# Kernel tuning notes

Hardware: AMD Instinct MI355X
Metric: run time of the kernel (lower is better)

Reference implementation:

```python
import jax, jax.numpy as jnp
import numpy as np

NUM_CLASSES = 80
ALPHA = 1.0
BETA = 6.0
EPS = 1e-9      # assigner eps
IOU_EPS = 1e-7  # bbox_iou eps


def _iou_xyxy(b1, b2):
    # b1: (B, A, 1, 4), b2: (B, 1, M, 4) -> IoU (B, A, M); matches bbox_iou(xywh=False)
    b1x1, b1y1, b1x2, b1y2 = (b1[..., 0], b1[..., 1], b1[..., 2], b1[..., 3])
    b2x1, b2y1, b2x2, b2y2 = (b2[..., 0], b2[..., 1], b2[..., 2], b2[..., 3])
    w1, h1 = b1x2 - b1x1, b1y2 - b1y1 + IOU_EPS
    w2, h2 = b2x2 - b2x1, b2y2 - b2y1 + IOU_EPS
    iw = jnp.clip(jnp.minimum(b1x2, b2x2) - jnp.maximum(b1x1, b2x1), 0)
    ih = jnp.clip(jnp.minimum(b1y2, b2y2) - jnp.maximum(b1y1, b2y1), 0)
    inter = iw * ih
    union = w1 * h1 + w2 * h2 - inter + IOU_EPS
    return inter / union


def _select_highest_overlaps(mask_pos, overlaps, M):
    # Always apply the dedup branch; it is a no-op when no anchor has >1 gt.
    fg = mask_pos.sum(-1)                                   # (B, A)
    multi = fg > 1
    is_max = jax.nn.one_hot(overlaps.argmax(-1), M, dtype=mask_pos.dtype)  # (B, A, M)
    mask_pos = jnp.where(multi[..., None], is_max, mask_pos)
    fg = mask_pos.sum(-1)
    tgt = mask_pos.argmax(-1).astype(jnp.int32)             # (B, A)
    return tgt, fg, mask_pos


def _forward(pd_scores, pd_bboxes, anc_points, gt_labels, gt_bboxes, mask_gt):
    B, A, C = pd_scores.shape
    M = gt_bboxes.shape[1]
    f = pd_scores.dtype
    mgt_b = mask_gt.astype(bool)                            # (B, M)
    mgt_f = mask_gt.astype(f)

    # --- box metrics ---
    overlaps = jnp.clip(_iou_xyxy(pd_bboxes[:, :, None, :], gt_bboxes[:, None, :, :]), 0)  # (B,A,M)
    idx = jnp.broadcast_to(gt_labels[:, None, :].astype(jnp.int32), (B, A, M))
    cls_scores = jnp.take_along_axis(pd_scores, idx, axis=-1)                              # (B,A,M)
    align_metric = cls_scores ** ALPHA * overlaps ** BETA

    # --- anchors inside gt boxes ---
    lt = anc_points[None, :, None, :] - gt_bboxes[:, None, :, :2]   # (B,A,M,2)
    rb = gt_bboxes[:, None, :, 2:] - anc_points[None, :, None, :]
    mask_in_gts = jnp.concatenate([lt, rb], -1).min(-1) > EPS       # (B,A,M) bool
    mask_pos = mask_in_gts.astype(f) * mgt_f[:, None, :]

    # --- fix 1 (vectorized: each (b,gt) iteration only touches its own column) ---
    need1 = mgt_b & (mask_pos.sum(1) == 0)                          # (B,M)
    has_in = mask_in_gts.any(1)                                     # (B,M)
    best1 = jnp.where(has_in, (overlaps * mask_in_gts).argmax(1), overlaps.argmax(1))  # (B,M)
    oh1 = jax.nn.one_hot(best1, A, dtype=f).transpose(0, 2, 1)      # (B,A,M)
    mask_pos = jnp.maximum(mask_pos, oh1 * need1[:, None, :].astype(f))

    tgt, fg, mask_pos = _select_highest_overlaps(mask_pos, overlaps, M)

    # --- fix 2: sequential per-gt reassignment (order-dependent -> lax.scan) ---
    anchor_ids = jnp.arange(A)
    gt_ids = jnp.arange(M)

    def step(carry, g):
        mp, tgi, fgm = carry
        assigned = jnp.any((fgm > 0) & (tgi == g), axis=1)          # (B,)
        need = jnp.take(mgt_b, g, axis=1) & (~assigned)             # (B,)
        best = jnp.take(overlaps, g, axis=2).argmax(1)              # (B,)
        oh_b = anchor_ids[None, :] == best[:, None]                 # (B,A) bool
        upd = need[:, None] & oh_b                                  # (B,A)
        col = (gt_ids == g)[None, None, :]
        mp = jnp.where(upd[:, :, None] & col, jnp.asarray(1, mp.dtype), mp)
        tgi = jnp.where(upd, g, tgi)
        fgm = jnp.where(upd, jnp.asarray(1, fgm.dtype), fgm)
        return (mp, tgi, fgm), None

    (mask_pos, tgt, fg), _ = jax.lax.scan(step, (mask_pos, tgt, fg), jnp.arange(M, dtype=jnp.int32))
    tgt, fg, mask_pos = _select_highest_overlaps(mask_pos, overlaps, M)

    # --- targets ---
    tl = jnp.take_along_axis(gt_labels.astype(jnp.int32), tgt, axis=1)   # (B,A)
    tl = jnp.clip(tl, 0, NUM_CLASSES)
    tb = jnp.take_along_axis(gt_bboxes, tgt[..., None], axis=1)          # (B,A,4)
    ts = jax.nn.one_hot(tl, C, dtype=f)                                  # (B,A,C)
    ts = jnp.where(fg[..., None] > 0, ts, jnp.asarray(0, f))

    # --- normalize scores by task-aligned metric ---
    am = align_metric * mask_pos
    pam = am.max(-1, keepdims=True)                                      # (B,A,1)
    pov = (overlaps * mask_pos).max(-1, keepdims=True)
    norm = (am * pov / (pam + EPS)).max(-1, keepdims=True)               # (B,A,1)
    ts = ts * norm
    return tl, tb, ts, fg > 0, tgt


def setup_inputs() -> dict:
    key = jax.random.key(0)
    B, C, M, IMG = 32, NUM_CLASSES, 32, 640
    ks = jax.random.split(key, 8)
    # YOLO-style anchor grid: strides 8/16/32 -> 80^2 + 40^2 + 20^2 = 8400 points
    pts = []
    for s in (8, 16, 32):
        n = IMG // s
        xs = (np.arange(n, dtype=np.float32) + 0.5) * s
        gy, gx = np.meshgrid(xs, xs, indexing="ij")
        pts.append(np.stack([gx.ravel(), gy.ravel()], -1))
    anc_points = jnp.asarray(np.concatenate(pts, 0))                     # (8400, 2)
    A = anc_points.shape[0]
    pd_scores = jax.random.uniform(ks[0], (B, A, C), dtype=jnp.float32)  # sigmoid-like scores
    wh_p = jax.random.uniform(ks[1], (B, A, 2), minval=16.0, maxval=256.0)
    ctr_p = anc_points[None] + jax.random.normal(ks[2], (B, A, 2)) * 8.0
    pd_bboxes = jnp.concatenate([ctr_p - wh_p / 2, ctr_p + wh_p / 2], -1)
    ctr_g = jax.random.uniform(ks[3], (B, M, 2), minval=60.0, maxval=580.0)
    wh_g = jax.random.uniform(ks[4], (B, M, 2), minval=24.0, maxval=240.0)
    gt_bboxes = jnp.concatenate([ctr_g - wh_g / 2, ctr_g + wh_g / 2], -1)
    gt_labels = jax.random.randint(ks[5], (B, M), 0, C, dtype=jnp.int32)
    n_gt = jax.random.randint(ks[6], (B, 1), 1, M + 1)
    mask_gt = jnp.arange(M)[None, :] < n_gt                              # (B, M) bool
    return dict(pd_scores=pd_scores, pd_bboxes=pd_bboxes, anc_points=anc_points,
                gt_labels=gt_labels, gt_bboxes=gt_bboxes, mask_gt=mask_gt)


def reference(pd_scores, pd_bboxes, anc_points, gt_labels, gt_bboxes, mask_gt):
    return _forward(pd_scores, pd_bboxes, anc_points, gt_labels, gt_bboxes, mask_gt)
```

## Files before the change

kernel.cpp:

```cpp
#include <hip/hip_runtime.h>


#define EPS_IN   1e-9f
#define IOU_EPS  1e-7f

__device__ __forceinline__ float iou_pair(const float4 p, const float4 g) {
#pragma clang fp contract(off)
    float w1 = p.z - p.x;
    float h1 = (p.w - p.y) + IOU_EPS;
    float w2 = g.z - g.x;
    float h2 = (g.w - g.y) + IOU_EPS;
    float iw = fminf(p.z, g.z) - fmaxf(p.x, g.x);
    iw = fmaxf(iw, 0.0f);
    float ih = fminf(p.w, g.w) - fmaxf(p.y, g.y);
    ih = fmaxf(ih, 0.0f);
    float inter = iw * ih;
    float uni = w1 * h1 + w2 * h2 - inter + IOU_EPS;
    float r = inter / uni;
    return fmaxf(r, 0.0f);
}

__device__ __forceinline__ int detect_mode(const void* mg, int nw) {
    const unsigned* w = (const unsigned*)mg;
    int lane = threadIdx.x & 63;
    int badI = 0, badF = 0;
    for (int i = lane; i < nw; i += 64) {
        unsigned v = w[i];
        badI |= (v > 1u);
        badF |= (v != 0u && v != 0x3F800000u);
    }
    unsigned long long bI = __ballot(badI != 0);
    unsigned long long bF = __ballot(badF != 0);
    return bI ? (bF ? 2 : 1) : 0;
}

__device__ __forceinline__ bool mask_at(const void* mg, int mode, int idx) {
    if (mode == 0) return ((const int*)mg)[idx] != 0;
    if (mode == 1) return ((const float*)mg)[idx] != 0.0f;
    return ((const unsigned char*)mg)[idx] != 0;
}

__global__ void k_phase1(const float4* __restrict__ pdb, const float2* __restrict__ anc,
                         const float4* __restrict__ gtb, const void* mg, int nw,
                         unsigned long long* __restrict__ colKey,
                         unsigned char* __restrict__ needByte,
                         unsigned* __restrict__ rowbits0, short* __restrict__ tgt0,
                         int* __restrict__ cntChunk,
                         int A, int M, int nCh) {
    int b = blockIdx.y, tid = threadIdx.x;
    int mode = detect_mode(mg, nw);
    size_t bA = (size_t)b * A;

    if ((int)blockIdx.x < M) {
        int m = blockIdx.x;
        if (!mask_at(mg, mode, b * M + m)) return;
        float4 g = gtb[b * M + m];
        unsigned long long key = 0ull;
        int hasin = 0;
        for (int a = tid; a < A; a += 256) {
            float v = iou_pair(pdb[bA + a], g);
            unsigned long long k =
                ((unsigned long long)__float_as_uint(v) << 32) | (0xFFFFFFFFu - (unsigned)a);
            if (k > key) key = k;
            float2 an = anc[a];
            float mn = fminf(fminf(an.x - g.x, an.y - g.y), fminf(g.z - an.x, g.w - an.y));
            hasin |= (mn > EPS_IN);
        }
        __shared__ unsigned long long skey[4];
        __shared__ int sin_[4];
        int lane = tid & 63, wid = tid >> 6;
        for (int off = 32; off; off >>= 1) {
            unsigned long long o = __shfl_down(key, off);
            if (o > key) key = o;
            hasin |= __shfl_down(hasin, off);
        }
        if (lane == 0) { skey[wid] = key; sin_[wid] = hasin; }
        __syncthreads();
        if (tid == 0) {
            for (int i = 1; i < 4; i++) { if (skey[i] > key) key = skey[i]; hasin |= sin_[i]; }
            colKey[b * M + m] = key;
            needByte[b * M + m] = hasin ? 0 : 1;
        }
    } else {
        int ch = blockIdx.x - M;
        int a = ch * 256 + tid;
        __shared__ float4 sg[32];
        __shared__ unsigned char smg[32];
        __shared__ int shist[32];
        if (tid < M) {
            sg[tid]  = gtb[b * M + tid];
            smg[tid] = mask_at(mg, mode, b * M + tid) ? 1 : 0;
        }
        if (tid < 32) shist[tid] = 0;
        __syncthreads();
        if (a < A) {
            float2 an = anc[a];
            unsigned bits = 0u;
            for (int m = 0; m < M; m++) {
                float4 g = sg[m];
                float mn = fminf(fminf(an.x - g.x, an.y - g.y), fminf(g.z - an.x, g.w - an.y));
                if (mn > EPS_IN && smg[m]) bits |= (1u << m);
            }
            rowbits0[bA + a] = bits;
            int pc = __popc(bits);
            int t;
            if (pc > 1) {
                float4 p = pdb[bA + a];
                float bv = -1.0f; int bm = 0;
                for (int m = 0; m < M; m++) {
                    float v = iou_pair(p, sg[m]);
                    if (v > bv) { bv = v; bm = m; }
                }
                t = bm;
            } else if (pc == 1) t = __ffs(bits) - 1;
            else t = -1;
            tgt0[bA + a] = (short)t;
            if (t >= 0) atomicAdd(&shist[t], 1);
        }
        __syncthreads();
        if (tid < 32) cntChunk[((size_t)b * nCh + ch) * 32 + tid] = shist[tid];
    }
}

__global__ void k_final(const float* __restrict__ pds, const float4* __restrict__ pdb,
                        const float4* __restrict__ gtb, const int* __restrict__ gtl,
                        const void* mg, int nw,
                        const unsigned long long* __restrict__ colKey,
                        const unsigned char* __restrict__ needByte,
                        const unsigned* __restrict__ rowbits0,
                        const short* __restrict__ tgt0,
                        const int* __restrict__ cntChunk,
                        float* __restrict__ out,
                        int A, int M, int C, int B, int nCh) {
    int b = blockIdx.y;
    int base = blockIdx.x * 256;
    int tid = threadIdx.x;
    int mode = detect_mode(mg, nw);
    size_t bA = (size_t)b * A;
    __shared__ float4 sg[32];
    __shared__ int slab[32];
    __shared__ int ovrA[64];
    __shared__ unsigned ovrBits[64];
    __shared__ int sNov;
    __shared__ float snorm[256];
    __shared__ int stl[256];
    if (tid < M) { sg[tid] = gtb[b * M + tid]; slab[tid] = gtl[b * M + tid]; }
    __syncthreads();

    if (tid < 64) {
        bool mv = false, needv = false;
        int best = -1, c0 = 0;
        if (tid < M) mv = mask_at(mg, mode, b * M + tid);
        if (mv) {
            unsigned long long key = colKey[b * M + tid];
            best = (int)(0xFFFFFFFFu - (unsigned)(key & 0xFFFFFFFFull));
            needv = (needByte[b * M + tid] != 0);
        }
        if (tid < 32) {
            for (int ch = 0; ch < nCh; ch++)
                c0 += cntChunk[((size_t)b * nCh + ch) * 32 + tid];
        }
        int myPre = (mv && best >= 0) ? (int)tgt0[bA + best] : -1;
        unsigned maskbits = (unsigned)__ballot(mv);
        unsigned needBits = (unsigned)__ballot(needv);
        unsigned myEq = 0u;
        for (int g2 = 0; g2 < 32; g2++) {
            int bb = __shfl(best, g2);
            if (bb == best) myEq |= (1u << g2);
        }
        int nov = 0;
        unsigned rem = needBits;
        while (rem) {
            int gl = __ffs(rem) - 1;
            unsigned em = __shfl(myEq, gl) & needBits;
            rem &= ~em;
            int aF = __shfl(best, gl);
            unsigned addb = em;
            unsigned bits0 = rowbits0[bA + aF];
            unsigned bits1 = bits0 | addb;
            int t1;
            if (__popc(bits1) > 1) {
                float4 p = pdb[bA + aF];
                unsigned long long kk = 0ull;
                if (tid < M) {
                    float v = iou_pair(p, sg[tid]);
                    kk = ((unsigned long long)__float_as_uint(v) << 32) |
                         (0xFFFFFFFFu - (unsigned)tid);
                }
                for (int off = 32; off; off >>= 1) {
                    unsigned long long o = __shfl_down(kk, off);
                    if (o > kk) kk = o;
                }
                kk = __shfl(kk, 0);
                t1 = (int)(0xFFFFFFFFu - (unsigned)(kk & 0xFFFFFFFFull));
            } else {
                t1 = __ffs(bits1) - 1;
            }
            int t0a = __shfl(myPre, gl);
            if (tid == t0a && t0a >= 0) c0--;
            if (tid == t1) c0++;
            if (best == aF) myPre = t1;
            if (tid == 0) { ovrA[nov] = aF; ovrBits[nov] = addb; }
            nov++;
        }
        unsigned applied = 0u;
        for (int g = 0; g < M; g++) {
            int cg = __shfl(c0, g);
            if (((maskbits >> g) & 1u) && cg == 0) {
                int aa      = __shfl(best, g);
                unsigned em = __shfl(myEq, g);
                unsigned x  = applied & em;
                int old;
                if (x) old = 31 - __clz(x);
                else   old = __shfl(myPre, g);
                if (tid == old) c0--;
                if (tid == g)   c0++;
                applied |= (1u << g);
                if (tid == 0) { ovrA[nov] = aa; ovrBits[nov] = 1u << g; }
                nov++;
            }
        }
        if (tid == 0) sNov = nov;
    }
    __syncthreads();

    int a = base + tid;
    size_t BA = (size_t)B * A;
    int nov = sNov;
    if (a < A) {
        size_t idx = bA + a;
        unsigned bits = rowbits0[idx];
        for (int j = 0; j < nov; j++)
            if (ovrA[j] == a) bits |= ovrBits[j];
        int pc = __popc(bits);
        int tgt, fg; float ov = 0.0f;
        float4 p = pdb[idx];
        if (pc > 1) {
            float bv = -1.0f; int bm = 0;
            for (int m = 0; m < M; m++) {
                float v = iou_pair(p, sg[m]);
                if (v > bv) { bv = v; bm = m; }
            }
            tgt = bm; fg = 1; ov = bv;
        } else if (pc == 1) {
            tgt = __ffs(bits) - 1; fg = 1;
            ov = iou_pair(p, sg[tgt]);
        } else { tgt = 0; fg = 0; }
        int lab = slab[tgt];
        int tl = min(max(lab, 0), C);
        float norm = 0.0f;
        if (fg) {
            int li = (lab >= 0 && lab < C) ? lab : 0;
            float cls = pds[idx * (size_t)C + li];
            float ov6 = powf(ov, 6.0f);
            float v = cls * ov6;
            norm = v * ov / (v + 1e-9f);
        }
        out[idx] = (float)tl;
        ((float4*)(out + BA))[idx] = sg[tgt];
        out[BA * (size_t)(5 + C) + idx] = fg ? 1.0f : 0.0f;
        out[BA * (size_t)(6 + C) + idx] = (float)tgt;
        snorm[tid] = norm;
        stl[tid] = tl;
    }
    __syncthreads();
    int cntA = min(256, A - base);
    int rowf4 = C >> 2;
    int nf4 = cntA * rowf4;
    float4* tsb = (float4*)(out + BA * 5 + (bA + base) * C);
    int q = 256 / rowf4, r = 256 - q * rowf4;
    int row = tid / rowf4;
    int c4  = tid - row * rowf4;
    for (int i = tid; i < nf4; i += 256) {
        float nv = snorm[row];
        int tl   = stl[row];
        int cb = c4 * 4;
        float4 v;
        v.x = (tl == cb + 0) ? nv : 0.0f;
        v.y = (tl == cb + 1) ? nv : 0.0f;
        v.z = (tl == cb + 2) ? nv : 0.0f;
        v.w = (tl == cb + 3) ? nv : 0.0f;
        tsb[i] = v;
        row += q; c4 += r;
        if (c4 >= rowf4) { c4 -= rowf4; row++; }
    }
}

extern "C" void kernel_launch(void* const* d_in, const int* in_sizes, int n_in,
                              void* d_out, int out_size, void* d_ws, size_t ws_size,
                              hipStream_t stream) {
    const float*  pd_scores = (const float*)d_in[0];
    const float4* pd_bboxes = (const float4*)d_in[1];
    const float2* anc       = (const float2*)d_in[2];
    const int*    gt_labels = (const int*)d_in[3];
    const float4* gt_bboxes = (const float4*)d_in[4];
    const void*   mask_gt   = d_in[5];

    int A = in_sizes[2] / 2;
    int B = in_sizes[1] / (A * 4);
    int M = in_sizes[3] / B;
    int C = (int)((long long)in_sizes[0] / ((long long)B * A));
    int nCh = (A + 255) / 256;
    int nw = (B * M) / 4; if (nw > 256) nw = 256;

    char* wp = (char*)d_ws;
    auto carve = [&](size_t bytes) -> char* {
        char* r = wp; wp += (bytes + 255) & ~(size_t)255; return r;
    };
    unsigned* rowbits0         = (unsigned*)carve((size_t)B * A * 4);
    short* tgt0                = (short*)carve((size_t)B * A * 2);
    unsigned long long* colKey = (unsigned long long*)carve((size_t)B * M * 8);
    unsigned char* needByte    = (unsigned char*)carve((size_t)B * M);
    int* cntChunk              = (int*)carve((size_t)B * nCh * 32 * 4);

    float* out = (float*)d_out;

    k_phase1<<<dim3(M + nCh, B), 256, 0, stream>>>(pd_bboxes, anc, gt_bboxes, mask_gt, nw,
                                                   colKey, needByte, rowbits0, tgt0,
                                                   cntChunk, A, M, nCh);
    k_final<<<dim3(nCh, B), 256, 0, stream>>>(pd_scores, pd_bboxes, gt_bboxes, gt_labels,
                                              mask_gt, nw, colKey, needByte, rowbits0,
                                              tgt0, cntChunk, out, A, M, C, B, nCh);
}
```

Measured before the change: 53.33 us.

## Fuse per-gt column argmax into anchor-chunk blocks and reuse target in final

Removes the separate per-gt blocks that each scanned all anchors. Every anchor-chunk block now computes all 32 IoUs once, keeps them in registers, and emits per-chunk column max keys and in-box bitmasks, which the final kernel reduces across chunks. The final kernel also reuses the stored tgt0 plus a small precomputed override table instead of recomputing the in-box bits and argmax per anchor. The cost is more wavefront reductions per chunk (32 shuffle-reduce loops), higher register pressure, and an extra serial reduction over chunks in the final kernel.

```diff
diff --git a/kernel.cpp b/kernel.cpp
--- a/kernel.cpp
+++ b/kernel.cpp
@@ -42,91 +42,95 @@
 
 __global__ void k_phase1(const float4* __restrict__ pdb, const float2* __restrict__ anc,
                          const float4* __restrict__ gtb, const void* mg, int nw,
-                         unsigned long long* __restrict__ colKey,
-                         unsigned char* __restrict__ needByte,
+                         unsigned long long* __restrict__ colChunk,
+                         unsigned* __restrict__ hasinChunk,
                          unsigned* __restrict__ rowbits0, short* __restrict__ tgt0,
                          int* __restrict__ cntChunk,
                          int A, int M, int nCh) {
-    int b = blockIdx.y, tid = threadIdx.x;
+    int b = blockIdx.y, ch = blockIdx.x, tid = threadIdx.x;
+    int lane = tid & 63, wid = tid >> 6;
     int mode = detect_mode(mg, nw);
+    __shared__ float4 sg[32];
+    __shared__ unsigned sMask;
+    __shared__ float swv[4][32];
+    __shared__ int   swa[4][32];
+    __shared__ unsigned swh[4];
+    __shared__ int shist[32];
+    if (tid < 32) {
+        sg[tid] = (tid < M) ? gtb[b * M + tid] : make_float4(0.f, 0.f, 0.f, 0.f);
+        shist[tid] = 0;
+    }
+    if (tid < 64) {
+        bool mv = (tid < M) && mask_at(mg, mode, b * M + tid);
+        unsigned mb = (unsigned)__ballot(mv);
+        if (tid == 0) sMask = mb;
+    }
+    __syncthreads();
+    unsigned maskb = sMask;
     size_t bA = (size_t)b * A;
-
-    if ((int)blockIdx.x < M) {
-        int m = blockIdx.x;
-        if (!mask_at(mg, mode, b * M + m)) return;
-        float4 g = gtb[b * M + m];
-        unsigned long long key = 0ull;
-        int hasin = 0;
-        for (int a = tid; a < A; a += 256) {
-            float v = iou_pair(pdb[bA + a], g);
-            unsigned long long k =
-                ((unsigned long long)__float_as_uint(v) << 32) | (0xFFFFFFFFu - (unsigned)a);
-            if (k > key) key = k;
-            float2 an = anc[a];
-            float mn = fminf(fminf(an.x - g.x, an.y - g.y), fminf(g.z - an.x, g.w - an.y));
-            hasin |= (mn > EPS_IN);
-        }
-        __shared__ unsigned long long skey[4];
-        __shared__ int sin_[4];
-        int lane = tid & 63, wid = tid >> 6;
-        for (int off = 32; off; off >>= 1) {
-            unsigned long long o = __shfl_down(key, off);
-            if (o > key) key = o;
-            hasin |= __shfl_down(hasin, off);
-        }
-        if (lane == 0) { skey[wid] = key; sin_[wid] = hasin; }
-        __syncthreads();
-        if (tid == 0) {
-            for (int i = 1; i < 4; i++) { if (skey[i] > key) key = skey[i]; hasin |= sin_[i]; }
-            colKey[b * M + m] = key;
-            needByte[b * M + m] = hasin ? 0 : 1;
-        }
-    } else {
-        int ch = blockIdx.x - M;
-        int a = ch * 256 + tid;
-        __shared__ float4 sg[32];
-        __shared__ unsigned char smg[32];
-        __shared__ int shist[32];
-        if (tid < M) {
-            sg[tid]  = gtb[b * M + tid];
-            smg[tid] = mask_at(mg, mode, b * M + tid) ? 1 : 0;
-        }
-        if (tid < 32) shist[tid] = 0;
-        __syncthreads();
-        if (a < A) {
-            float2 an = anc[a];
-            unsigned bits = 0u;
-            for (int m = 0; m < M; m++) {
-                float4 g = sg[m];
-                float mn = fminf(fminf(an.x - g.x, an.y - g.y), fminf(g.z - an.x, g.w - an.y));
-                if (mn > EPS_IN && smg[m]) bits |= (1u << m);
-            }
-            rowbits0[bA + a] = bits;
-            int pc = __popc(bits);
-            int t;
-            if (pc > 1) {
-                float4 p = pdb[bA + a];
-                float bv = -1.0f; int bm = 0;
-                for (int m = 0; m < M; m++) {
-                    float v = iou_pair(p, sg[m]);
-                    if (v > bv) { bv = v; bm = m; }
-                }
-                t = bm;
-            } else if (pc == 1) t = __ffs(bits) - 1;
-            else t = -1;
-            tgt0[bA + a] = (short)t;
-            if (t >= 0) atomicAdd(&shist[t], 1);
-        }
-        __syncthreads();
-        if (tid < 32) cntChunk[((size_t)b * nCh + ch) * 32 + tid] = shist[tid];
+    int a = ch * 256 + tid;
+    bool valid = a < A;
+    float4 p = make_float4(0.f, 0.f, 0.f, 0.f);
+    float2 an = make_float2(0.f, 0.f);
+    if (valid) { p = pdb[bA + a]; an = anc[a]; }
+    float v[32];
+    unsigned inbox = 0u;
+#pragma unroll
+    for (int m = 0; m < 32; m++) {
+        float4 g = sg[m];
+        bool ok = valid && (m < M);
+        v[m] = ok ? iou_pair(p, g) : -1.0f;
+        float mn = fminf(fminf(an.x - g.x, an.y - g.y), fminf(g.z - an.x, g.w - an.y));
+        if (ok && mn > EPS_IN) inbox |= (1u << m);
+    }
+    if (valid) {
+        unsigned bits = inbox & maskb;
+        int pc = __popc(bits);
+        int t = -1;
+        if (pc > 1) {
+            float bv = -0.5f; int bm = 0;
+#pragma unroll
+            for (int m = 0; m < 32; m++) { if (v[m] > bv) { bv = v[m]; bm = m; } }
+            t = bm;
+        } else if (pc == 1) t = __ffs(bits) - 1;
+        rowbits0[bA + a] = bits;
+        tgt0[bA + a] = (short)t;
+        if (t >= 0) atomicAdd(&shist[t], 1);
+    } else if (a < ((A + 255) & ~255)) {
+    }
+    unsigned hw = inbox;
+    for (int off = 32; off; off >>= 1) hw |= __shfl_xor(hw, off);
+    if (lane == 0) swh[wid] = hw;
+#pragma unroll
+    for (int m = 0; m < 32; m++) {
+        float vm = v[m];
+        for (int off = 32; off; off >>= 1) vm = fmaxf(vm, __shfl_xor(vm, off));
+        unsigned long long eq = __ballot(v[m] == vm);
+        if (lane == 0) {
+            swv[wid][m] = vm;
+            swa[wid][m] = ch * 256 + wid * 64 + (__ffsll((unsigned long long)eq) - 1);
+        }
+    }
+    __syncthreads();
+    if (tid < 32) {
+        float bv = swv[0][tid]; int ba = swa[0][tid];
+        for (int w = 1; w < 4; w++) {
+            float vv = swv[w][tid]; int aa = swa[w][tid];
+            if (vv > bv || (vv == bv && aa < ba)) { bv = vv; ba = aa; }
+        }
+        unsigned long long key = (bv < 0.0f) ? 0ull :
+            (((unsigned long long)__float_as_uint(bv) << 32) | (0xFFFFFFFFu - (unsigned)ba));
+        colChunk[((size_t)b * nCh + ch) * 32 + tid] = key;
+        cntChunk[((size_t)b * nCh + ch) * 32 + tid] = shist[tid];
+        if (tid == 0) hasinChunk[b * nCh + ch] = swh[0] | swh[1] | swh[2] | swh[3];
     }
 }
 
 __global__ void k_final(const float* __restrict__ pds, const float4* __restrict__ pdb,
                         const float4* __restrict__ gtb, const int* __restrict__ gtl,
                         const void* mg, int nw,
-                        const unsigned long long* __restrict__ colKey,
-                        const unsigned char* __restrict__ needByte,
+                        const unsigned long long* __restrict__ colChunk,
+                        const unsigned* __restrict__ hasinChunk,
                         const unsigned* __restrict__ rowbits0,
                         const short* __restrict__ tgt0,
                         const int* __restrict__ cntChunk,
@@ -140,27 +144,32 @@
     __shared__ float4 sg[32];
     __shared__ int slab[32];
     __shared__ int ovrA[64];
-    __shared__ unsigned ovrBits[64];
+    __shared__ unsigned ovrAdd[64];
+    __shared__ short ovrT[64];
     __shared__ int sNov;
     __shared__ float snorm[256];
     __shared__ int stl[256];
-    if (tid < M) { sg[tid] = gtb[b * M + tid]; slab[tid] = gtl[b * M + tid]; }
+    if (tid < 32) {
+        sg[tid]   = (tid < M) ? gtb[b * M + tid] : make_float4(0.f, 0.f, 0.f, 0.f);
+        slab[tid] = (tid < M) ? gtl[b * M + tid] : 0;
+    }
     __syncthreads();
 
     if (tid < 64) {
-        bool mv = false, needv = false;
-        int best = -1, c0 = 0;
-        if (tid < M) mv = mask_at(mg, mode, b * M + tid);
-        if (mv) {
-            unsigned long long key = colKey[b * M + tid];
-            best = (int)(0xFFFFFFFFu - (unsigned)(key & 0xFFFFFFFFull));
-            needv = (needByte[b * M + tid] != 0);
-        }
+        bool mv = (tid < M) && mask_at(mg, mode, b * M + tid);
+        unsigned long long key = 0ull;
+        int c0 = 0; unsigned horAll = 0u;
         if (tid < 32) {
-            for (int ch = 0; ch < nCh; ch++)
+            for (int ch = 0; ch < nCh; ch++) {
+                unsigned long long k2 = colChunk[((size_t)b * nCh + ch) * 32 + tid];
+                if (k2 > key) key = k2;
                 c0 += cntChunk[((size_t)b * nCh + ch) * 32 + tid];
-        }
-        int myPre = (mv && best >= 0) ? (int)tgt0[bA + best] : -1;
+                horAll |= hasinChunk[b * nCh + ch];
+            }
+        }
+        int best = mv ? (int)(0xFFFFFFFFu - (unsigned)(key & 0xFFFFFFFFull)) : -1;
+        bool needv = mv && !((horAll >> tid) & 1u);
+        int myPre = (best >= 0) ? (int)tgt0[bA + best] : -1;
         unsigned maskbits = (unsigned)__ballot(mv);
         unsigned needBits = (unsigned)__ballot(needv);
         unsigned myEq = 0u;
@@ -176,15 +185,14 @@
             rem &= ~em;
             int aF = __shfl(best, gl);
             unsigned addb = em;
-            unsigned bits0 = rowbits0[bA + aF];
-            unsigned bits1 = bits0 | addb;
+            unsigned bits1 = rowbits0[bA + aF] | addb;
             int t1;
             if (__popc(bits1) > 1) {
                 float4 p = pdb[bA + aF];
                 unsigned long long kk = 0ull;
                 if (tid < M) {
-                    float v = iou_pair(p, sg[tid]);
-                    kk = ((unsigned long long)__float_as_uint(v) << 32) |
+                    float vv = iou_pair(p, sg[tid]);
+                    kk = ((unsigned long long)__float_as_uint(vv) << 32) |
                          (0xFFFFFFFFu - (unsigned)tid);
                 }
                 for (int off = 32; off; off >>= 1) {
@@ -200,7 +208,7 @@
             if (tid == t0a && t0a >= 0) c0--;
             if (tid == t1) c0++;
             if (best == aF) myPre = t1;
-            if (tid == 0) { ovrA[nov] = aF; ovrBits[nov] = addb; }
+            if (tid == 0) { ovrA[nov] = aF; ovrAdd[nov] = addb; }
             nov++;
         }
         unsigned applied = 0u;
@@ -216,50 +224,68 @@
                 if (tid == old) c0--;
                 if (tid == g)   c0++;
                 applied |= (1u << g);
-                if (tid == 0) { ovrA[nov] = aa; ovrBits[nov] = 1u << g; }
+                if (tid == 0) { ovrA[nov] = aa; ovrAdd[nov] = 1u << g; }
                 nov++;
             }
         }
         if (tid == 0) sNov = nov;
     }
     __syncthreads();
+    if (tid < 64) {
+        int nov2 = sNov;
+        for (int j = 0; j < nov2; j++) {
+            int aj = ovrA[j];
+            unsigned addT = 0u;
+            for (int k = 0; k < nov2; k++) if (ovrA[k] == aj) addT |= ovrAdd[k];
+            unsigned bt = rowbits0[bA + aj] | addT;
+            int tf;
+            if (__popc(bt) > 1) {
+                float4 p = pdb[bA + aj];
+                unsigned long long kk = 0ull;
+                if (tid < M) {
+                    float vv = iou_pair(p, sg[tid]);
+                    kk = ((unsigned long long)__float_as_uint(vv) << 32) |
+                         (0xFFFFFFFFu - (unsigned)tid);
+                }
+                for (int off = 32; off; off >>= 1) {
+                    unsigned long long o = __shfl_down(kk, off);
+                    if (o > kk) kk = o;
+                }
+                kk = __shfl(kk, 0);
+                tf = (int)(0xFFFFFFFFu - (unsigned)(kk & 0xFFFFFFFFull));
+            } else {
+                tf = __ffs(bt) - 1;
+            }
+            if (tid == 0) ovrT[j] = (short)tf;
+        }
+    }
+    __syncthreads();
 
     int a = base + tid;
     size_t BA = (size_t)B * A;
-    int nov = sNov;
     if (a < A) {
         size_t idx = bA + a;
-        unsigned bits = rowbits0[idx];
-        for (int j = 0; j < nov; j++)
-            if (ovrA[j] == a) bits |= ovrBits[j];
-        int pc = __popc(bits);
-        int tgt, fg; float ov = 0.0f;
-        float4 p = pdb[idx];
-        if (pc > 1) {
-            float bv = -1.0f; int bm = 0;
-            for (int m = 0; m < M; m++) {
-                float v = iou_pair(p, sg[m]);
-                if (v > bv) { bv = v; bm = m; }
-            }
-            tgt = bm; fg = 1; ov = bv;
-        } else if (pc == 1) {
-            tgt = __ffs(bits) - 1; fg = 1;
-            ov = iou_pair(p, sg[tgt]);
-        } else { tgt = 0; fg = 0; }
-        int lab = slab[tgt];
+        int t = (int)tgt0[idx];
+        int nov2 = sNov;
+        for (int j = 0; j < nov2; j++)
+            if (ovrA[j] == a) t = (int)ovrT[j];
+        int fg = (t >= 0);
+        int tgtO = fg ? t : 0;
+        int lab = slab[tgtO];
         int tl = min(max(lab, 0), C);
         float norm = 0.0f;
         if (fg) {
+            float ov = iou_pair(pdb[idx], sg[t]);
             int li = (lab >= 0 && lab < C) ? lab : 0;
             float cls = pds[idx * (size_t)C + li];
             float ov6 = powf(ov, 6.0f);
-            float v = cls * ov6;
-            norm = v * ov / (v + 1e-9f);
+            float vv = cls * ov6;
+            norm = vv * ov / (vv + 1e-9f);
         }
         out[idx] = (float)tl;
-        ((float4*)(out + BA))[idx] = sg[tgt];
+        ((float4*)(out + BA))[idx] = sg[tgtO];
         out[BA * (size_t)(5 + C) + idx] = fg ? 1.0f : 0.0f;
-        out[BA * (size_t)(6 + C) + idx] = (float)tgt;
+        out[BA * (size_t)(6 + C) + idx] = (float)tgtO;
         snorm[tid] = norm;
         stl[tid] = tl;
     }
@@ -275,12 +301,12 @@
         float nv = snorm[row];
         int tl   = stl[row];
         int cb = c4 * 4;
-        float4 v;
-        v.x = (tl == cb + 0) ? nv : 0.0f;
-        v.y = (tl == cb + 1) ? nv : 0.0f;
-        v.z = (tl == cb + 2) ? nv : 0.0f;
-        v.w = (tl == cb + 3) ? nv : 0.0f;
-        tsb[i] = v;
+        float4 vv;
+        vv.x = (tl == cb + 0) ? nv : 0.0f;
+        vv.y = (tl == cb + 1) ? nv : 0.0f;
+        vv.z = (tl == cb + 2) ? nv : 0.0f;
+        vv.w = (tl == cb + 3) ? nv : 0.0f;
+        tsb[i] = vv;
         row += q; c4 += r;
         if (c4 >= rowf4) { c4 -= rowf4; row++; }
     }
@@ -309,16 +335,17 @@
     };
     unsigned* rowbits0         = (unsigned*)carve((size_t)B * A * 4);
     short* tgt0                = (short*)carve((size_t)B * A * 2);
-    unsigned long long* colKey = (unsigned long long*)carve((size_t)B * M * 8);
-    unsigned char* needByte    = (unsigned char*)carve((size_t)B * M);
+    unsigned long long* colChunk = (unsigned long long*)carve((size_t)B * nCh * 32 * 8);
+    unsigned* hasinChunk       = (unsigned*)carve((size_t)B * nCh * 4);
     int* cntChunk              = (int*)carve((size_t)B * nCh * 32 * 4);
 
     float* out = (float*)d_out;
 
-    k_phase1<<<dim3(M + nCh, B), 256, 0, stream>>>(pd_bboxes, anc, gt_bboxes, mask_gt, nw,
-                                                   colKey, needByte, rowbits0, tgt0,
-                                                   cntChunk, A, M, nCh);
+    k_phase1<<<dim3(nCh, B), 256, 0, stream>>>(pd_bboxes, anc, gt_bboxes, mask_gt, nw,
+                                               colChunk, hasinChunk, rowbits0, tgt0,
+                                               cntChunk, A, M, nCh);
     k_final<<<dim3(nCh, B), 256, 0, stream>>>(pd_scores, pd_bboxes, gt_bboxes, gt_labels,
-                                              mask_gt, nw, colKey, needByte, rowbits0,
-                                              tgt0, cntChunk, out, A, M, C, B, nCh);
-}
+                                              mask_gt, nw, colChunk, hasinChunk,
+                                              rowbits0, tgt0, cntChunk, out,
+                                              A, M, C, B, nCh);
+}
```

After: 91.25 us. +71.1%, slower.
